# Performance work log

Hardware: AMD Instinct MI355X
Metric: run time of the kernel (lower is better)

The kernel has to match this reference:

```python
import jax, jax.numpy as jnp
import numpy as np
from jax import lax

B, T, HID = 1, 2048, 2048
HQ, HKV, D = 16, 2, 128
G = HQ // HKV
KERNEL, SELECT, TOPN, WIN = 32, 64, 16, 512
SCALE = D ** -0.5
NEG = -1e30


def rotate_half(x):
    h = x.shape[-1] // 2
    return jnp.concatenate([-x[..., h:], x[..., :h]], axis=-1)


def apply_rope(x, cos, sin):
    # x: [B,T,H,D]; cos/sin: [T,D]
    c = cos[None, :, None, :]
    s = sin[None, :, None, :]
    return x * c + rotate_half(x) * s


def masked_attend(q, k, v, mask):
    # q,k,v: [B,T,H,D]; mask broadcastable to [B,H,T,T]
    scores = jnp.einsum('bthd,bshd->bhts', q, k) * SCALE
    scores = jnp.where(mask, scores, NEG)
    p = jax.nn.softmax(scores, axis=-1) * mask
    return jnp.einsum('bhts,bshd->bthd', p, v)


def setup_inputs() -> dict:
    key = jax.random.key(0)
    ks = jax.random.split(key, 12)
    hidden_states = jax.random.normal(ks[0], (B, T, HID), dtype=jnp.float32)
    # RoPE tables
    inv_freq = 1.0 / (10000.0 ** (jnp.arange(0, D, 2, dtype=jnp.float32) / D))
    freqs = jnp.arange(T, dtype=jnp.float32)[:, None] * inv_freq[None, :]
    emb = jnp.concatenate([freqs, freqs], axis=-1)
    cos, sin = jnp.cos(emb), jnp.sin(emb)
    std = 0.02
    Wq = jax.random.normal(ks[1], (HQ * D, HID), jnp.float32) * std
    bq = jax.random.normal(ks[2], (HQ * D,), jnp.float32) * std
    Wk = jax.random.normal(ks[3], (HKV * D, HID), jnp.float32) * std
    bk = jax.random.normal(ks[4], (HKV * D,), jnp.float32) * std
    Wv = jax.random.normal(ks[5], (HKV * D, HID), jnp.float32) * std
    bv = jax.random.normal(ks[6], (HKV * D,), jnp.float32) * std
    Wo = jax.random.normal(ks[7], (HID, HQ * D), jnp.float32) * std
    w_ck = 1.0 / KERNEL + jax.random.normal(ks[8], (KERNEL,), jnp.float32) * std
    w_cv = 1.0 / KERNEL + jax.random.normal(ks[9], (KERNEL,), jnp.float32) * std
    Wg = jax.random.normal(ks[10], (HQ, D, 3), jnp.float32) * std
    return dict(hidden_states=hidden_states, cos=cos, sin=sin, Wq=Wq, bq=bq,
                Wk=Wk, bk=bk, Wv=Wv, bv=bv, Wo=Wo, w_ck=w_ck, w_cv=w_cv, Wg=Wg)


def nsa_forward(hidden_states, cos, sin, Wq, bq, Wk, bk, Wv, bv, Wo, w_ck, w_cv, Wg):
    q = (hidden_states @ Wq.T + bq).reshape(B, T, HQ, D)
    k = (hidden_states @ Wk.T + bk).reshape(B, T, HKV, D)
    v = (hidden_states @ Wv.T + bv).reshape(B, T, HKV, D)
    q = apply_rope(q, cos, sin)
    k = apply_rope(k, cos, sin)
    k_rep = jnp.repeat(k, G, axis=2)  # [B,T,HQ,D]
    v_rep = jnp.repeat(v, G, axis=2)

    t_ar = jnp.arange(T)
    causal = t_ar[:, None] >= t_ar[None, :]  # [T,T]

    # ---- compressed branch (stride == kernel) ----
    Nc = T // KERNEL
    kb = k.reshape(B, Nc, KERNEL, HKV, D)
    vb = v.reshape(B, Nc, KERNEL, HKV, D)
    k_cmp = jnp.einsum('bnkhd,k->bnhd', kb, w_ck)
    v_cmp = jnp.einsum('bnkhd,k->bnhd', vb, w_cv)
    k_cmp_rep = jnp.repeat(k_cmp, G, axis=2)  # [B,Nc,HQ,D]
    v_cmp_rep = jnp.repeat(v_cmp, G, axis=2)
    n_ar = jnp.arange(Nc)
    cmp_mask = t_ar[:, None] >= (n_ar[None, :] + 1) * KERNEL - 1  # block fully past
    sc = jnp.einsum('bthd,bnhd->bhtn', q, k_cmp_rep) * SCALE
    sc = jnp.where(cmp_mask[None, None], sc, NEG)
    p_cmp = jax.nn.softmax(sc, axis=-1) * cmp_mask[None, None]  # [B,HQ,T,Nc]
    o_cmp = jnp.einsum('bhtn,bnhd->bthd', p_cmp, v_cmp_rep)

    # ---- block selection from compressed scores (shared within KV group) ----
    S = T // SELECT
    ratio = SELECT // KERNEL
    p_kv = p_cmp.reshape(B, HKV, G, T, Nc).sum(axis=2)  # [B,HKV,T,Nc]
    blk_score = p_kv.reshape(B, HKV, T, S, ratio).sum(axis=-1)  # [B,HKV,T,S]
    s_ar = jnp.arange(S)
    cur_blk = t_ar // SELECT
    force = (jax.nn.one_hot(cur_blk, S) + (s_ar[None, :] == 0)) > 0  # [T,S]
    bonus = force.astype(jnp.float32) * 1e6  # always keep first + current block
    vis = (s_ar * SELECT)[None, :] <= t_ar[:, None]  # [T,S]
    blk_score = jnp.where(vis[None, None], blk_score + bonus[None, None], NEG)
    _, idx = lax.top_k(blk_score, TOPN)  # [B,HKV,T,TOPN]
    sel_blk = jax.nn.one_hot(idx, S).sum(axis=-2) > 0  # [B,HKV,T,S]
    sel_key = jnp.repeat(sel_blk, SELECT, axis=-1)  # [B,HKV,T,T]
    sel_mask = sel_key & causal[None, None]
    sel_mask = jnp.repeat(sel_mask, G, axis=1)  # [B,HQ,T,T]
    o_sel = masked_attend(q, k_rep, v_rep, sel_mask)

    # ---- sliding window branch ----
    win_mask = causal & (t_ar[:, None] - t_ar[None, :] < WIN)
    o_win = masked_attend(q, k_rep, v_rep, win_mask[None, None])

    # ---- gated combine ----
    g = jax.nn.sigmoid(jnp.einsum('bthd,hde->bthe', q, Wg))  # [B,T,HQ,3]
    o = g[..., 0:1] * o_cmp + g[..., 1:2] * o_sel + g[..., 2:3] * o_win
    return o.reshape(B, T, HQ * D) @ Wo.T


def reference(hidden_states, cos, sin, Wq, bq, Wk, bk, Wv, bv, Wo, w_ck, w_cv, Wg):
    return nsa_forward(hidden_states, cos, sin, Wq, bq, Wk, bk, Wv, bv, Wo, w_ck, w_cv, Wg)
```

## Files before the change

### kernel.cpp

```cpp
#include <hip/hip_runtime.h>
#include <hip/hip_bf16.h>

constexpr int T = 2048, HID = 2048;
constexpr int HQ = 16, HKV = 2, D = 128, G = 8;
constexpr int KER = 32, SEL = 64, TOPN = 16, WIN = 512;
constexpr int NC = T / KER;
constexpr int S  = T / SEL;
constexpr float SCALE = 0.08838834764831845f;
constexpr float NEGF = -1e30f;

typedef __attribute__((ext_vector_type(8))) __bf16 bf16x8;
typedef __attribute__((ext_vector_type(4))) float f32x4;

__device__ __forceinline__ ushort f2bf(float f) {
    __hip_bfloat16 h = __float2bfloat16(f);
    return *reinterpret_cast<const ushort*>(&h);
}

__global__ void to_bf16_kernel(const float* __restrict__ in, ushort* __restrict__ out, int n4) {
    int i = blockIdx.x * 256 + threadIdx.x;
    if (i >= n4) return;
    float4 f = *reinterpret_cast<const float4*>(&in[(size_t)i * 4]);
    ushort4 u;
    u.x = f2bf(f.x); u.y = f2bf(f.y); u.z = f2bf(f.z); u.w = f2bf(f.w);
    *reinterpret_cast<ushort4*>(&out[(size_t)i * 4]) = u;
}

template<int OUT_MODE, bool HAS_BIAS>
__global__ __launch_bounds__(256)
void gemm_mfma(const ushort* __restrict__ A, const ushort* __restrict__ B,
               const float* __restrict__ bias, float* __restrict__ C,
               int M, int N, int K) {
    __shared__ ushort As[128][40];
    __shared__ ushort Bs[128][40];
    const int m0 = blockIdx.y * 128, n0 = blockIdx.x * 128;
    const int tid = threadIdx.x;
    const int w = tid >> 6, lane = tid & 63;
    const int wr = (w >> 1) * 64, wc = (w & 1) * 64;
    const int lx = lane & 15, lg = lane >> 4;
    f32x4 acc[4][4];
#pragma unroll
    for (int mi = 0; mi < 4; ++mi)
#pragma unroll
        for (int ni = 0; ni < 4; ++ni)
#pragma unroll
            for (int j = 0; j < 4; ++j) acc[mi][ni][j] = 0.f;

    for (int k0 = 0; k0 < K; k0 += 32) {
        {
            int r = tid >> 1, half = (tid & 1) * 16;
            const ushort* ap = A + (size_t)(m0 + r) * K + k0 + half;
            const ushort* bp = B + (size_t)(n0 + r) * K + k0 + half;
            *reinterpret_cast<uint4*>(&As[r][half])     = *reinterpret_cast<const uint4*>(ap);
            *reinterpret_cast<uint4*>(&As[r][half + 8]) = *reinterpret_cast<const uint4*>(ap + 8);
            *reinterpret_cast<uint4*>(&Bs[r][half])     = *reinterpret_cast<const uint4*>(bp);
            *reinterpret_cast<uint4*>(&Bs[r][half + 8]) = *reinterpret_cast<const uint4*>(bp + 8);
        }
        __syncthreads();
        bf16x8 af[4], bfr[4];
#pragma unroll
        for (int mi = 0; mi < 4; ++mi)
            af[mi] = *reinterpret_cast<const bf16x8*>(&As[wr + mi * 16 + lx][lg * 8]);
#pragma unroll
        for (int ni = 0; ni < 4; ++ni)
            bfr[ni] = *reinterpret_cast<const bf16x8*>(&Bs[wc + ni * 16 + lx][lg * 8]);
#pragma unroll
        for (int mi = 0; mi < 4; ++mi)
#pragma unroll
            for (int ni = 0; ni < 4; ++ni)
                acc[mi][ni] = __builtin_amdgcn_mfma_f32_16x16x32_bf16(af[mi], bfr[ni], acc[mi][ni], 0, 0, 0);
        __syncthreads();
    }
#pragma unroll
    for (int mi = 0; mi < 4; ++mi)
#pragma unroll
        for (int ni = 0; ni < 4; ++ni)
#pragma unroll
            for (int j = 0; j < 4; ++j) {
                int m = m0 + wr + mi * 16 + lg * 4 + j;
                int n = n0 + wc + ni * 16 + lx;
                float val = acc[mi][ni][j];
                if (HAS_BIAS) val += bias[n];
                if (OUT_MODE == 1) val = __bfloat162float(__float2bfloat16(val));
                C[(size_t)m * N + n] = val;
            }
}

__global__ void rope_kernel(float* __restrict__ x, const float* __restrict__ cosb,
                            const float* __restrict__ sinb, int H) {
    int idx = blockIdx.x * blockDim.x + threadIdx.x;
    if (idx >= T * H * 64) return;
    int d = idx & 63;
    int th = idx >> 6;
    int h = th % H, t = th / H;
    float c0 = cosb[t * D + d],      s0 = sinb[t * D + d];
    float c1 = cosb[t * D + d + 64], s1 = sinb[t * D + d + 64];
    float* p = x + ((size_t)t * H + h) * D;
    float x0 = p[d], x1 = p[d + 64];
    p[d]      = x0 * c0 - x1 * s0;
    p[d + 64] = x1 * c1 + x0 * s1;
}

__global__ void compress_kernel(const float* __restrict__ k, const float* __restrict__ v,
                                const float* __restrict__ wck, const float* __restrict__ wcv,
                                float* __restrict__ k_cmp, float* __restrict__ v_cmp) {
    int idx = blockIdx.x * blockDim.x + threadIdx.x;
    if (idx >= NC * HKV * D) return;
    int d = idx % D;
    int h = (idx / D) % HKV;
    int n = idx / (D * HKV);
    float ak = 0.f, av = 0.f;
#pragma unroll 8
    for (int j = 0; j < KER; ++j) {
        size_t off = ((size_t)(n * KER + j) * HKV + h) * D + d;
        ak += k[off] * wck[j];
        av += v[off] * wcv[j];
    }
    k_cmp[idx] = ak;
    v_cmp[idx] = av;
}

__global__ __launch_bounds__(256)
void cmp_attn_wave(const float* __restrict__ q, const float* __restrict__ k_cmp,
                   const float* __restrict__ v_cmp, float* __restrict__ p_cmp,
                   float* __restrict__ o_cmp) {
    int wid = blockIdx.x * 4 + (threadIdx.x >> 6);
    int lane = threadIdx.x & 63;
    int t = wid / HQ, h = wid % HQ;
    int kh = h / G;
    int n = lane;
    bool vis = (t >= KER * n + KER - 1);
    const float4* qp = reinterpret_cast<const float4*>(q + ((size_t)t * HQ + h) * D);
    const float4* kp = reinterpret_cast<const float4*>(k_cmp + ((size_t)n * HKV + kh) * D);
    float a0 = 0.f, a1 = 0.f, a2 = 0.f, a3 = 0.f;
#pragma unroll
    for (int i = 0; i < 8; ++i) {
        float4 x0 = qp[i * 4 + 0], y0 = kp[i * 4 + 0];
        float4 x1 = qp[i * 4 + 1], y1 = kp[i * 4 + 1];
        float4 x2 = qp[i * 4 + 2], y2 = kp[i * 4 + 2];
        float4 x3 = qp[i * 4 + 3], y3 = kp[i * 4 + 3];
        a0 += x0.x * y0.x + x0.y * y0.y + x0.z * y0.z + x0.w * y0.w;
        a1 += x1.x * y1.x + x1.y * y1.y + x1.z * y1.z + x1.w * y1.w;
        a2 += x2.x * y2.x + x2.y * y2.y + x2.z * y2.z + x2.w * y2.w;
        a3 += x3.x * y3.x + x3.y * y3.y + x3.z * y3.z + x3.w * y3.w;
    }
    float acc = (a0 + a1) + (a2 + a3);
    float s = vis ? acc * SCALE : NEGF;
    float mx = s;
#pragma unroll
    for (int off = 32; off; off >>= 1) mx = fmaxf(mx, __shfl_xor(mx, off));
    float e = vis ? expf(s - mx) : 0.f;
    float sum = e;
#pragma unroll
    for (int off = 32; off; off >>= 1) sum += __shfl_xor(sum, off);
    float p = (sum > 0.f) ? (e / sum) : 0.f;
    p_cmp[((size_t)h * T + t) * NC + n] = p;
    float c00 = 0.f, c01 = 0.f, c02 = 0.f, c03 = 0.f;
    float c10 = 0.f, c11 = 0.f, c12 = 0.f, c13 = 0.f;
    int d0 = lane, d1 = lane + 64;
    for (int nn = 0; nn < NC; nn += 4) {
        float p0 = __shfl(p, nn), p1 = __shfl(p, nn + 1);
        float p2 = __shfl(p, nn + 2), p3 = __shfl(p, nn + 3);
        const float* v0 = v_cmp + ((size_t)(nn + 0) * HKV + kh) * D;
        const float* v1 = v_cmp + ((size_t)(nn + 1) * HKV + kh) * D;
        const float* v2 = v_cmp + ((size_t)(nn + 2) * HKV + kh) * D;
        const float* v3 = v_cmp + ((size_t)(nn + 3) * HKV + kh) * D;
        c00 += p0 * v0[d0]; c10 += p0 * v0[d1];
        c01 += p1 * v1[d0]; c11 += p1 * v1[d1];
        c02 += p2 * v2[d0]; c12 += p2 * v2[d1];
        c03 += p3 * v3[d0]; c13 += p3 * v3[d1];
    }
    float* op = o_cmp + ((size_t)t * HQ + h) * D;
    op[d0] = (c00 + c01) + (c02 + c03);
    op[d1] = (c10 + c11) + (c12 + c13);
}

__global__ void select_kernel(const float* __restrict__ p_cmp, unsigned* __restrict__ selmask) {
    int idx = blockIdx.x * blockDim.x + threadIdx.x;
    if (idx >= HKV * T) return;
    int t = idx % T, kh = idx / T;
    float bs[S];
#pragma unroll
    for (int s = 0; s < S; ++s) bs[s] = 0.f;
    for (int g = 0; g < G; ++g) {
        const float* pp = p_cmp + (((size_t)(kh * G + g)) * T + t) * NC;
#pragma unroll
        for (int s = 0; s < S; ++s) bs[s] += pp[2 * s] + pp[2 * s + 1];
    }
    int cur = t / SEL;
#pragma unroll
    for (int s = 0; s < S; ++s) {
        bool vis = (s * SEL <= t);
        bool force = (s == 0) || (s == cur);
        bs[s] = vis ? (bs[s] + (force ? 1e6f : 0.f)) : NEGF;
    }
    unsigned chosen = 0;
    for (int it = 0; it < TOPN; ++it) {
        float best = -3e38f;
        int bj = 0;
#pragma unroll
        for (int s = 0; s < S; ++s) {
            bool free_s = !((chosen >> s) & 1);
            if (free_s && bs[s] > best) { best = bs[s]; bj = s; }
        }
        chosen |= 1u << bj;
    }
    selmask[idx] = chosen;
}

__global__ __launch_bounds__(512)
void attn_mfma(const float* __restrict__ qf, const ushort* __restrict__ kb,
               const ushort* __restrict__ vb, const unsigned* __restrict__ selmask,
               float* __restrict__ o_sel, float* __restrict__ o_win) {
    const int mode = blockIdx.y;
    const int kh = blockIdx.x >> 7;
    const int tt = blockIdx.x & 127;
    const int t0 = tt * 16;
    const int w = threadIdx.x >> 6;
    const int lane = threadIdx.x & 63;
    const int h = kh * G + w;
    const int lx = lane & 15;
    const int lg = lane >> 4;
    const int koff = lg * 8;

    __shared__ ushort VT[128][72];
    __shared__ ushort Pl[8][16][72];

    bf16x8 aq[4];
    {
        const float* qrow = qf + ((size_t)(t0 + lx) * HQ + h) * D;
#pragma unroll
        for (int s4 = 0; s4 < 4; ++s4) {
            union { bf16x8 v; ushort u[8]; } tmp;
#pragma unroll
            for (int jj = 0; jj < 8; ++jj) tmp.u[jj] = f2bf(qrow[s4 * 32 + koff + jj]);
            aq[s4] = tmp.v;
        }
    }
    unsigned mskj[4] = {0, 0, 0, 0};
    unsigned un = 0;
    if (mode == 0) {
#pragma unroll
        for (int j = 0; j < 4; ++j) {
            mskj[j] = selmask[kh * T + t0 + lg * 4 + j];
            un |= mskj[j];
        }
        un |= __shfl_xor(un, 16);
        un |= __shfl_xor(un, 32);
    }
    int smax = (t0 + 15) / 64;
    int smin = 0;
    if (mode == 1) {
        int lo = t0 - (WIN - 1);
        if (lo < 0) lo = 0;
        smin = lo / 64;
    }

    float m_run[4], l_run[4];
    f32x4 oacc[8];
#pragma unroll
    for (int j = 0; j < 4; ++j) { m_run[j] = NEGF; l_run[j] = 0.f; }
#pragma unroll
    for (int ds = 0; ds < 8; ++ds)
#pragma unroll
        for (int j = 0; j < 4; ++j) oacc[ds][j] = 0.f;

    for (int s = smin; s <= smax; ++s) {
        if (mode == 0 && !((un >> s) & 1u)) continue;
        __syncthreads();
        {
            int i = threadIdx.x;
            int key = i >> 3;
            int d0 = (i & 7) * 16;
            const ushort* src = vb + ((size_t)(s * 64 + key) * HKV + kh) * D + d0;
            union { uint4 q; ushort u[8]; } r0, r1;
            r0.q = *reinterpret_cast<const uint4*>(src);
            r1.q = *reinterpret_cast<const uint4*>(src + 8);
            int kcol = key ^ (((d0 >> 4) & 7) << 3);
#pragma unroll
            for (int e = 0; e < 8; ++e) VT[d0 + e][kcol] = r0.u[e];
#pragma unroll
            for (int e = 0; e < 8; ++e) VT[d0 + 8 + e][kcol] = r1.u[e];
        }
        __syncthreads();
        f32x4 sc[4];
#pragma unroll
        for (int ks = 0; ks < 4; ++ks)
#pragma unroll
            for (int j = 0; j < 4; ++j) sc[ks][j] = 0.f;
#pragma unroll
        for (int ks = 0; ks < 4; ++ks) {
            const ushort* kbase = kb + ((size_t)(s * 64 + ks * 16 + lx) * HKV + kh) * D;
#pragma unroll
            for (int s4 = 0; s4 < 4; ++s4) {
                bf16x8 bk = *reinterpret_cast<const bf16x8*>(kbase + s4 * 32 + koff);
                sc[ks] = __builtin_amdgcn_mfma_f32_16x16x32_bf16(aq[s4], bk, sc[ks], 0, 0, 0);
            }
        }
#pragma unroll
        for (int ks = 0; ks < 4; ++ks) {
            int key = s * 64 + ks * 16 + lx;
#pragma unroll
            for (int j = 0; j < 4; ++j) {
                int trow = t0 + lg * 4 + j;
                bool valid = (key <= trow) &&
                             (mode ? (key >= trow - (WIN - 1)) : (((mskj[j] >> s) & 1u) != 0));
                sc[ks][j] = valid ? sc[ks][j] * SCALE : NEGF;
            }
        }
#pragma unroll
        for (int j = 0; j < 4; ++j) {
            float mj = fmaxf(fmaxf(sc[0][j], sc[1][j]), fmaxf(sc[2][j], sc[3][j]));
            mj = fmaxf(mj, __shfl_xor(mj, 1));
            mj = fmaxf(mj, __shfl_xor(mj, 2));
            mj = fmaxf(mj, __shfl_xor(mj, 4));
            mj = fmaxf(mj, __shfl_xor(mj, 8));
            float mn = fmaxf(m_run[j], mj);
            float scl = expf(m_run[j] - mn);
            l_run[j] *= scl;
#pragma unroll
            for (int ds = 0; ds < 8; ++ds) oacc[ds][j] *= scl;
            float rs = 0.f;
#pragma unroll
            for (int ks = 0; ks < 4; ++ks) {
                float x = sc[ks][j];
                float p = (x < -1e29f) ? 0.f : expf(x - mn);
                sc[ks][j] = p;
                rs += p;
            }
            rs += __shfl_xor(rs, 1);
            rs += __shfl_xor(rs, 2);
            rs += __shfl_xor(rs, 4);
            rs += __shfl_xor(rs, 8);
            l_run[j] += rs;
            m_run[j] = mn;
        }
#pragma unroll
        for (int ks = 0; ks < 4; ++ks)
#pragma unroll
            for (int j = 0; j < 4; ++j)
                Pl[w][lg * 4 + j][ks * 16 + lx] = f2bf(sc[ks][j]);
        __syncthreads();
#pragma unroll
        for (int sl = 0; sl < 2; ++sl) {
            bf16x8 ap = *reinterpret_cast<const bf16x8*>(&Pl[w][lx][sl * 32 + koff]);
#pragma unroll
            for (int ds = 0; ds < 8; ++ds) {
                int col = (sl * 32 + koff) ^ (ds << 3);
                bf16x8 bv = *reinterpret_cast<const bf16x8*>(&VT[ds * 16 + lx][col]);
                oacc[ds] = __builtin_amdgcn_mfma_f32_16x16x32_bf16(ap, bv, oacc[ds], 0, 0, 0);
            }
        }
    }
    float* optr = mode ? o_win : o_sel;
    float inv[4];
#pragma unroll
    for (int j = 0; j < 4; ++j) inv[j] = 1.f / l_run[j];
#pragma unroll
    for (int ds = 0; ds < 8; ++ds)
#pragma unroll
        for (int j = 0; j < 4; ++j) {
            int row = lg * 4 + j;
            int d = ds * 16 + lx;
            optr[((size_t)(t0 + row) * HQ + h) * D + d] = oacc[ds][j] * inv[j];
        }
}

__global__ __launch_bounds__(256)
void gate_wave(const float* __restrict__ q, const float* __restrict__ Wg,
               const float* __restrict__ o_cmp, const float* __restrict__ o_sel,
               const float* __restrict__ o_win, float* __restrict__ o_comb) {
    int wid = blockIdx.x * 4 + (threadIdx.x >> 6);
    int lane = threadIdx.x & 63;
    int t = wid / HQ, h = wid % HQ;
    const float* qp = q + ((size_t)t * HQ + h) * D;
    const float* wg = Wg + (size_t)h * D * 3;
    float g0 = 0.f, g1 = 0.f, g2 = 0.f;
#pragma unroll
    for (int r = 0; r < 2; ++r) {
        int d = lane + r * 64;
        float qv = qp[d];
        g0 += qv * wg[d * 3 + 0];
        g1 += qv * wg[d * 3 + 1];
        g2 += qv * wg[d * 3 + 2];
    }
#pragma unroll
    for (int off = 32; off; off >>= 1) {
        g0 += __shfl_xor(g0, off);
        g1 += __shfl_xor(g1, off);
        g2 += __shfl_xor(g2, off);
    }
    g0 = 1.f / (1.f + expf(-g0));
    g1 = 1.f / (1.f + expf(-g1));
    g2 = 1.f / (1.f + expf(-g2));
    size_t base = ((size_t)t * HQ + h) * D;
#pragma unroll
    for (int r = 0; r < 2; ++r) {
        size_t i = base + lane + r * 64;
        o_comb[i] = g0 * o_cmp[i] + g1 * o_sel[i] + g2 * o_win[i];
    }
}

extern "C" void kernel_launch(void* const* d_in, const int* in_sizes, int n_in,
                              void* d_out, int out_size, void* d_ws, size_t ws_size,
                              hipStream_t stream) {
    const float* hs   = (const float*)d_in[0];
    const float* cosb = (const float*)d_in[1];
    const float* sinb = (const float*)d_in[2];
    const float* Wq   = (const float*)d_in[3];
    const float* bq   = (const float*)d_in[4];
    const float* Wk   = (const float*)d_in[5];
    const float* bk   = (const float*)d_in[6];
    const float* Wv   = (const float*)d_in[7];
    const float* bv   = (const float*)d_in[8];
    const float* Wo   = (const float*)d_in[9];
    const float* w_ck = (const float*)d_in[10];
    const float* w_cv = (const float*)d_in[11];
    const float* Wg   = (const float*)d_in[12];
    float* out = (float*)d_out;

    float* ws = (float*)d_ws;
    size_t off = 0;
    float* q      = ws + off; off += (size_t)T * HQ * D;
    float* k      = ws + off; off += (size_t)T * HKV * D;
    float* v      = ws + off; off += (size_t)T * HKV * D;
    float* k_cmp  = ws + off; off += (size_t)NC * HKV * D;
    float* v_cmp  = ws + off; off += (size_t)NC * HKV * D;
    float* p_cmp  = ws + off; off += (size_t)HQ * T * NC;
    float* o_cmp  = ws + off; off += (size_t)T * HQ * D;
    float* o_sel  = ws + off; off += (size_t)T * HQ * D;
    float* o_win  = ws + off; off += (size_t)T * HQ * D;
    unsigned* selmask = (unsigned*)(ws + off); off += HKV * T;
    ushort* kb = (ushort*)(ws + off);
    ushort* vb = kb + (size_t)T * HKV * D;

    ushort* hs_b = (ushort*)p_cmp;
    ushort* Wq_b = (ushort*)o_cmp;
    ushort* Wk_b = (ushort*)o_sel;
    ushort* Wv_b = Wk_b + (size_t)HKV * D * HID;
    ushort* Wo_b = (ushort*)o_sel;
    ushort* oc_b = (ushort*)o_win;

    const int NQ = HQ * D, NKVd = HKV * D;

    to_bf16_kernel<<<(T * HID / 4) / 256, 256, 0, stream>>>(hs, hs_b, T * HID / 4);
    to_bf16_kernel<<<(NQ * HID / 4) / 256, 256, 0, stream>>>(Wq, Wq_b, NQ * HID / 4);
    to_bf16_kernel<<<(NKVd * HID / 4) / 256, 256, 0, stream>>>(Wk, Wk_b, NKVd * HID / 4);
    to_bf16_kernel<<<(NKVd * HID / 4) / 256, 256, 0, stream>>>(Wv, Wv_b, NKVd * HID / 4);
    gemm_mfma<0, true><<<dim3(NQ / 128, T / 128), 256, 0, stream>>>(hs_b, Wq_b, bq, q, T, NQ, HID);
    gemm_mfma<0, true><<<dim3(NKVd / 128, T / 128), 256, 0, stream>>>(hs_b, Wk_b, bk, k, T, NKVd, HID);
    gemm_mfma<0, true><<<dim3(NKVd / 128, T / 128), 256, 0, stream>>>(hs_b, Wv_b, bv, v, T, NKVd, HID);
    rope_kernel<<<(T * HQ * 64) / 256, 256, 0, stream>>>(q, cosb, sinb, HQ);
    rope_kernel<<<(T * HKV * 64) / 256, 256, 0, stream>>>(k, cosb, sinb, HKV);
    to_bf16_kernel<<<(T * HKV * D / 4 + 255) / 256, 256, 0, stream>>>(k, kb, T * HKV * D / 4);
    to_bf16_kernel<<<(T * HKV * D / 4 + 255) / 256, 256, 0, stream>>>(v, vb, T * HKV * D / 4);
    compress_kernel<<<(NC * HKV * D) / 256, 256, 0, stream>>>(k, v, w_ck, w_cv, k_cmp, v_cmp);
    cmp_attn_wave<<<(T * HQ) / 4, 256, 0, stream>>>(q, k_cmp, v_cmp, p_cmp, o_cmp);
    select_kernel<<<(HKV * T) / 256, 256, 0, stream>>>(p_cmp, selmask);
    attn_mfma<<<dim3(HKV * (T / 16), 2), 512, 0, stream>>>(q, kb, vb, selmask, o_sel, o_win);
    gate_wave<<<(T * HQ) / 4, 256, 0, stream>>>(q, Wg, o_cmp, o_sel, o_win, o_cmp);
    to_bf16_kernel<<<(T * NQ / 4) / 256, 256, 0, stream>>>(o_cmp, oc_b, T * NQ / 4);
    to_bf16_kernel<<<(HID * NQ / 4) / 256, 256, 0, stream>>>(Wo, Wo_b, HID * NQ / 4);
    gemm_mfma<1, false><<<dim3(HID / 128, T / 128), 256, 0, stream>>>(oc_b, Wo_b, nullptr, out, T, HID, NQ);
}
```

Measured before the change: 728.4 us.

## Fuse selected and window attention into one pass with shared K/V tiles

```diff
diff --git a/kernel.cpp b/kernel.cpp
--- a/kernel.cpp
+++ b/kernel.cpp
@@ -176,7 +176,7 @@
 }
 
 __global__ void select_kernel(const float* __restrict__ p_cmp, unsigned* __restrict__ selmask) {
-    int idx = blockIdx.x * blockDim.x + threadIdx.x;
+    int idx = blockIdx.x * 64 + threadIdx.x;
     if (idx >= HKV * T) return;
     int t = idx % T, kh = idx / T;
     float bs[S];
@@ -208,23 +208,35 @@
     selmask[idx] = chosen;
 }
 
-__global__ __launch_bounds__(512)
-void attn_mfma(const float* __restrict__ qf, const ushort* __restrict__ kb,
-               const ushort* __restrict__ vb, const unsigned* __restrict__ selmask,
-               float* __restrict__ o_sel, float* __restrict__ o_win) {
-    const int mode = blockIdx.y;
-    const int kh = blockIdx.x >> 7;
-    const int tt = blockIdx.x & 127;
+__global__ void transpose_v(const ushort* __restrict__ vb, ushort* __restrict__ vbt) {
+    __shared__ ushort tl[32][33];
+    int kh = blockIdx.z, t0 = blockIdx.x * 32, d0 = blockIdx.y * 32;
+    int tx = threadIdx.x, ty = threadIdx.y;
+    for (int r = ty; r < 32; r += 8)
+        tl[r][tx] = vb[(size_t)(t0 + r) * (HKV * D) + kh * D + d0 + tx];
+    __syncthreads();
+    for (int r = ty; r < 32; r += 8)
+        vbt[((size_t)kh * D + d0 + r) * T + t0 + tx] = tl[tx][r];
+}
+
+__global__ __launch_bounds__(256)
+void attn_fused(const float* __restrict__ qf, const ushort* __restrict__ kb,
+                const ushort* __restrict__ vbt, const unsigned* __restrict__ selmask,
+                float* __restrict__ o_sel, float* __restrict__ o_win) {
+    const int bid = blockIdx.x;
+    const int kh = bid >> 8;
+    const int rest = bid & 255;
+    const int hh = rest >> 7;
+    const int tt = rest & 127;
     const int t0 = tt * 16;
     const int w = threadIdx.x >> 6;
     const int lane = threadIdx.x & 63;
-    const int h = kh * G + w;
-    const int lx = lane & 15;
-    const int lg = lane >> 4;
-    const int koff = lg * 8;
-
+    const int h = kh * G + hh * 4 + w;
+    const int lx = lane & 15, lg = lane >> 4, koff = lg * 8;
+
+    __shared__ ushort Ks[64][136];
     __shared__ ushort VT[128][72];
-    __shared__ ushort Pl[8][16][72];
+    __shared__ ushort Pl[4][16][72];
 
     bf16x8 aq[4];
     {
@@ -237,132 +249,130 @@
             aq[s4] = tmp.v;
         }
     }
-    unsigned mskj[4] = {0, 0, 0, 0};
+    unsigned mskj[4];
     unsigned un = 0;
-    if (mode == 0) {
-#pragma unroll
-        for (int j = 0; j < 4; ++j) {
-            mskj[j] = selmask[kh * T + t0 + lg * 4 + j];
-            un |= mskj[j];
-        }
-        un |= __shfl_xor(un, 16);
-        un |= __shfl_xor(un, 32);
-    }
-    int smax = (t0 + 15) / 64;
-    int smin = 0;
-    if (mode == 1) {
-        int lo = t0 - (WIN - 1);
-        if (lo < 0) lo = 0;
-        smin = lo / 64;
-    }
-
-    float m_run[4], l_run[4];
-    f32x4 oacc[8];
-#pragma unroll
-    for (int j = 0; j < 4; ++j) { m_run[j] = NEGF; l_run[j] = 0.f; }
+#pragma unroll
+    for (int j = 0; j < 4; ++j) {
+        mskj[j] = selmask[kh * T + t0 + lg * 4 + j];
+        un |= mskj[j];
+    }
+    un |= __shfl_xor(un, 16);
+    un |= __shfl_xor(un, 32);
+
+    int wlo_t = t0 - (WIN - 1); if (wlo_t < 0) wlo_t = 0;
+    const int swin_min = wlo_t / 64;
+    const int smax = (t0 + 15) / 64;
+
+    float msel[4], lsel[4], mwin[4], lwin[4];
+    f32x4 osel[8], owin[8];
+#pragma unroll
+    for (int j = 0; j < 4; ++j) { msel[j] = NEGF; lsel[j] = 0.f; mwin[j] = NEGF; lwin[j] = 0.f; }
 #pragma unroll
     for (int ds = 0; ds < 8; ++ds)
 #pragma unroll
-        for (int j = 0; j < 4; ++j) oacc[ds][j] = 0.f;
-
-    for (int s = smin; s <= smax; ++s) {
-        if (mode == 0 && !((un >> s) & 1u)) continue;
+        for (int j = 0; j < 4; ++j) { osel[ds][j] = 0.f; owin[ds][j] = 0.f; }
+
+    for (int s = 0; s <= smax; ++s) {
+        const bool selA = (un >> s) & 1u;
+        const bool winA = (s >= swin_min);
+        if (!selA && !winA) continue;
         __syncthreads();
         {
-            int i = threadIdx.x;
-            int key = i >> 3;
-            int d0 = (i & 7) * 16;
-            const ushort* src = vb + ((size_t)(s * 64 + key) * HKV + kh) * D + d0;
-            union { uint4 q; ushort u[8]; } r0, r1;
-            r0.q = *reinterpret_cast<const uint4*>(src);
-            r1.q = *reinterpret_cast<const uint4*>(src + 8);
-            int kcol = key ^ (((d0 >> 4) & 7) << 3);
-#pragma unroll
-            for (int e = 0; e < 8; ++e) VT[d0 + e][kcol] = r0.u[e];
-#pragma unroll
-            for (int e = 0; e < 8; ++e) VT[d0 + 8 + e][kcol] = r1.u[e];
+            int row = threadIdx.x >> 2, seg = threadIdx.x & 3;
+            const ushort* src = kb + ((size_t)(s * 64 + row) * HKV + kh) * D + seg * 32;
+            uint4* dst = reinterpret_cast<uint4*>(&Ks[row][seg * 32]);
+            const uint4* sp = reinterpret_cast<const uint4*>(src);
+            dst[0] = sp[0]; dst[1] = sp[1]; dst[2] = sp[2]; dst[3] = sp[3];
+        }
+        {
+            int row = threadIdx.x >> 1, seg = threadIdx.x & 1;
+            const ushort* src = vbt + ((size_t)kh * D + row) * T + s * 64 + seg * 32;
+            uint4* dst = reinterpret_cast<uint4*>(&VT[row][seg * 32]);
+            const uint4* sp = reinterpret_cast<const uint4*>(src);
+            dst[0] = sp[0]; dst[1] = sp[1]; dst[2] = sp[2]; dst[3] = sp[3];
         }
         __syncthreads();
         f32x4 sc[4];
 #pragma unroll
-        for (int ks = 0; ks < 4; ++ks)
+        for (int ks = 0; ks < 4; ++ks) {
 #pragma unroll
             for (int j = 0; j < 4; ++j) sc[ks][j] = 0.f;
 #pragma unroll
-        for (int ks = 0; ks < 4; ++ks) {
-            const ushort* kbase = kb + ((size_t)(s * 64 + ks * 16 + lx) * HKV + kh) * D;
-#pragma unroll
             for (int s4 = 0; s4 < 4; ++s4) {
-                bf16x8 bk = *reinterpret_cast<const bf16x8*>(kbase + s4 * 32 + koff);
+                bf16x8 bk = *reinterpret_cast<const bf16x8*>(&Ks[ks * 16 + lx][s4 * 32 + koff]);
                 sc[ks] = __builtin_amdgcn_mfma_f32_16x16x32_bf16(aq[s4], bk, sc[ks], 0, 0, 0);
             }
         }
-#pragma unroll
-        for (int ks = 0; ks < 4; ++ks) {
-            int key = s * 64 + ks * 16 + lx;
+        auto run_mode = [&](float* m_run, float* l_run, f32x4* oa, bool isWin) {
+            float pv[4][4];
+#pragma unroll
+            for (int ks = 0; ks < 4; ++ks) {
+                int key = s * 64 + ks * 16 + lx;
+#pragma unroll
+                for (int j = 0; j < 4; ++j) {
+                    int trow = t0 + lg * 4 + j;
+                    bool valid = (key <= trow) &&
+                                 (isWin ? (key >= trow - (WIN - 1)) : (((mskj[j] >> s) & 1u) != 0));
+                    pv[ks][j] = valid ? sc[ks][j] * SCALE : NEGF;
+                }
+            }
 #pragma unroll
             for (int j = 0; j < 4; ++j) {
-                int trow = t0 + lg * 4 + j;
-                bool valid = (key <= trow) &&
-                             (mode ? (key >= trow - (WIN - 1)) : (((mskj[j] >> s) & 1u) != 0));
-                sc[ks][j] = valid ? sc[ks][j] * SCALE : NEGF;
+                float mj = fmaxf(fmaxf(pv[0][j], pv[1][j]), fmaxf(pv[2][j], pv[3][j]));
+                mj = fmaxf(mj, __shfl_xor(mj, 1));
+                mj = fmaxf(mj, __shfl_xor(mj, 2));
+                mj = fmaxf(mj, __shfl_xor(mj, 4));
+                mj = fmaxf(mj, __shfl_xor(mj, 8));
+                float mn = fmaxf(m_run[j], mj);
+                float scl = expf(m_run[j] - mn);
+                l_run[j] *= scl;
+#pragma unroll
+                for (int ds = 0; ds < 8; ++ds) oa[ds][j] *= scl;
+                float rs = 0.f;
+#pragma unroll
+                for (int ks = 0; ks < 4; ++ks) {
+                    float x = pv[ks][j];
+                    float p = (x < -1e29f) ? 0.f : expf(x - mn);
+                    pv[ks][j] = p;
+                    rs += p;
+                }
+                rs += __shfl_xor(rs, 1);
+                rs += __shfl_xor(rs, 2);
+                rs += __shfl_xor(rs, 4);
+                rs += __shfl_xor(rs, 8);
+                l_run[j] += rs;
+                m_run[j] = mn;
             }
-        }
-#pragma unroll
-        for (int j = 0; j < 4; ++j) {
-            float mj = fmaxf(fmaxf(sc[0][j], sc[1][j]), fmaxf(sc[2][j], sc[3][j]));
-            mj = fmaxf(mj, __shfl_xor(mj, 1));
-            mj = fmaxf(mj, __shfl_xor(mj, 2));
-            mj = fmaxf(mj, __shfl_xor(mj, 4));
-            mj = fmaxf(mj, __shfl_xor(mj, 8));
-            float mn = fmaxf(m_run[j], mj);
-            float scl = expf(m_run[j] - mn);
-            l_run[j] *= scl;
-#pragma unroll
-            for (int ds = 0; ds < 8; ++ds) oacc[ds][j] *= scl;
-            float rs = 0.f;
-#pragma unroll
-            for (int ks = 0; ks < 4; ++ks) {
-                float x = sc[ks][j];
-                float p = (x < -1e29f) ? 0.f : expf(x - mn);
-                sc[ks][j] = p;
-                rs += p;
+#pragma unroll
+            for (int ks = 0; ks < 4; ++ks)
+#pragma unroll
+                for (int j = 0; j < 4; ++j)
+                    Pl[w][lg * 4 + j][ks * 16 + lx] = f2bf(pv[ks][j]);
+#pragma unroll
+            for (int sl = 0; sl < 2; ++sl) {
+                bf16x8 ap = *reinterpret_cast<const bf16x8*>(&Pl[w][lx][sl * 32 + koff]);
+#pragma unroll
+                for (int ds = 0; ds < 8; ++ds) {
+                    bf16x8 bv = *reinterpret_cast<const bf16x8*>(&VT[ds * 16 + lx][sl * 32 + koff]);
+                    oa[ds] = __builtin_amdgcn_mfma_f32_16x16x32_bf16(ap, bv, oa[ds], 0, 0, 0);
+                }
             }
-            rs += __shfl_xor(rs, 1);
-            rs += __shfl_xor(rs, 2);
-            rs += __shfl_xor(rs, 4);
-            rs += __shfl_xor(rs, 8);
-            l_run[j] += rs;
-            m_run[j] = mn;
-        }
-#pragma unroll
-        for (int ks = 0; ks < 4; ++ks)
-#pragma unroll
-            for (int j = 0; j < 4; ++j)
-                Pl[w][lg * 4 + j][ks * 16 + lx] = f2bf(sc[ks][j]);
-        __syncthreads();
-#pragma unroll
-        for (int sl = 0; sl < 2; ++sl) {
-            bf16x8 ap = *reinterpret_cast<const bf16x8*>(&Pl[w][lx][sl * 32 + koff]);
-#pragma unroll
-            for (int ds = 0; ds < 8; ++ds) {
-                int col = (sl * 32 + koff) ^ (ds << 3);
-                bf16x8 bv = *reinterpret_cast<const bf16x8*>(&VT[ds * 16 + lx][col]);
-                oacc[ds] = __builtin_amdgcn_mfma_f32_16x16x32_bf16(ap, bv, oacc[ds], 0, 0, 0);
-            }
-        }
-    }
-    float* optr = mode ? o_win : o_sel;
-    float inv[4];
-#pragma unroll
-    for (int j = 0; j < 4; ++j) inv[j] = 1.f / l_run[j];
+        };
+        if (selA) run_mode(msel, lsel, osel, false);
+        if (winA) run_mode(mwin, lwin, owin, true);
+    }
+    float isel[4], iwin[4];
+#pragma unroll
+    for (int j = 0; j < 4; ++j) { isel[j] = 1.f / lsel[j]; iwin[j] = 1.f / lwin[j]; }
 #pragma unroll
     for (int ds = 0; ds < 8; ++ds)
 #pragma unroll
         for (int j = 0; j < 4; ++j) {
             int row = lg * 4 + j;
             int d = ds * 16 + lx;
-            optr[((size_t)(t0 + row) * HQ + h) * D + d] = oacc[ds][j] * inv[j];
+            size_t o = ((size_t)(t0 + row) * HQ + h) * D + d;
+            o_sel[o] = osel[ds][j] * isel[j];
+            o_win[o] = owin[ds][j] * iwin[j];
         }
 }
 
@@ -438,6 +448,7 @@
     ushort* Wq_b = (ushort*)o_cmp;
     ushort* Wk_b = (ushort*)o_sel;
     ushort* Wv_b = Wk_b + (size_t)HKV * D * HID;
+    ushort* vbt  = (ushort*)p_cmp;
     ushort* Wo_b = (ushort*)o_sel;
     ushort* oc_b = (ushort*)o_win;
 
@@ -456,8 +467,9 @@
     to_bf16_kernel<<<(T * HKV * D / 4 + 255) / 256, 256, 0, stream>>>(v, vb, T * HKV * D / 4);
     compress_kernel<<<(NC * HKV * D) / 256, 256, 0, stream>>>(k, v, w_ck, w_cv, k_cmp, v_cmp);
     cmp_attn_wave<<<(T * HQ) / 4, 256, 0, stream>>>(q, k_cmp, v_cmp, p_cmp, o_cmp);
-    select_kernel<<<(HKV * T) / 256, 256, 0, stream>>>(p_cmp, selmask);
-    attn_mfma<<<dim3(HKV * (T / 16), 2), 512, 0, stream>>>(q, kb, vb, selmask, o_sel, o_win);
+    select_kernel<<<(HKV * T) / 64, 64, 0, stream>>>(p_cmp, selmask);
+    transpose_v<<<dim3(T / 32, D / 32, HKV), dim3(32, 8), 0, stream>>>(vb, vbt);
+    attn_fused<<<HKV * 2 * (T / 16), 256, 0, stream>>>(q, kb, vbt, selmask, o_sel, o_win);
     gate_wave<<<(T * HQ) / 4, 256, 0, stream>>>(q, Wg, o_cmp, o_sel, o_win, o_cmp);
     to_bf16_kernel<<<(T * NQ / 4) / 256, 256, 0, stream>>>(o_cmp, oc_b, T * NQ / 4);
     to_bf16_kernel<<<(HID * NQ / 4) / 256, 256, 0, stream>>>(Wo, Wo_b, HID * NQ / 4);
```

Result: faster. 692.0 us (-5.0%).
